# Performance work log

Measured on AMD Instinct MI355X. Metric: run time of the kernel, lower is better.

The kernel has to match this reference:

```python
import jax, jax.numpy as jnp
import numpy as np

GAMMA = 0.1
BUDGET = 64
EPS = 1e-8  # torch cosine_similarity clamp


def setup_inputs() -> dict:
    key = jax.random.key(0)
    k1, k2, k3, k4 = jax.random.split(key, 4)
    num_nodes, feat_dim, num_cand = 100000, 256, 50000
    return {
        "influence_scores": jax.random.normal(k1, (num_cand,), dtype=jnp.float32),
        "node_features": jax.random.normal(k2, (num_nodes, feat_dim), dtype=jnp.float32),
        "candidate_indices": jax.random.randint(k3, (num_cand,), 0, num_nodes, dtype=jnp.int64),
        "injected_feat": jax.random.normal(k4, (feat_dim,), dtype=jnp.float32),
    }


def reference(influence_scores, node_features, candidate_indices, injected_feat):
    # gather candidate features: [num_cand, feat_dim]
    cand_feat = node_features[candidate_indices]
    # cosine similarity vs injected_feat, torch-style eps clamp on norms
    inj_norm = jnp.maximum(jnp.linalg.norm(injected_feat), EPS)
    cand_norm = jnp.maximum(jnp.linalg.norm(cand_feat, axis=-1), EPS)
    sim_penalty = (cand_feat @ injected_feat) / (cand_norm * inj_norm)
    edge_scores = influence_scores - GAMMA * sim_penalty
    top_k = min(BUDGET, candidate_indices.shape[0])
    _, selected_indices = jax.lax.top_k(edge_scores, top_k)
    return candidate_indices[selected_indices], edge_scores
```

## Files before the change

kernel.cpp:

```cpp
#include <hip/hip_runtime.h>
#include <hip/hip_bf16.h>
#include <float.h>
#include <limits.h>

#define FEAT       256
#define GAMMA_F    0.1f
#define EPS_F      1e-8f
#define KSEL       64
#define NBUCK      4096
#define KSHIFT     20
#define NB1        1024
#define NB3        64
#define CPW        4
#define BCAP       64
#define CAP        4096
#define ZWORDS     (NBUCK + NB3 + 3)

__device__ __forceinline__ unsigned key_of(float v) {
    unsigned u = __float_as_uint(v);
    return u ^ ((u >> 31) ? 0xFFFFFFFFu : 0x80000000u);
}

__device__ __forceinline__ bool comes_first(float va, int ia, float vb, int ib) {
    return (va > vb) || (va == vb && ia < ib);
}

__global__ __launch_bounds__(256) void edge_score_kernel(
    const float* __restrict__ infl,
    const float* __restrict__ feats,
    const int*   __restrict__ cand,
    const float* __restrict__ inj,
    float*       __restrict__ scores,
    unsigned*    __restrict__ ws_zero,
    int num_cand)
{
    const int gtid = blockIdx.x * blockDim.x + threadIdx.x;
    if (gtid < ZWORDS) ws_zero[gtid] = 0u;

    const int lane    = threadIdx.x & 63;
    const int wid     = gtid >> 6;
    const int nwaves  = NB1 * 4;
    const int ngroups = (num_cand + CPW - 1) / CPW;

    const float4 g = *reinterpret_cast<const float4*>(inj + lane * 4);
    float ng = g.x * g.x + g.y * g.y + g.z * g.z + g.w * g.w;
    #pragma unroll
    for (int off = 32; off > 0; off >>= 1) ng += __shfl_xor(ng, off);
    const float inj_n = fmaxf(sqrtf(ng), EPS_F);

    for (int grp = wid; grp < ngroups; grp += nwaves) {
        const int base   = grp * CPW;
        const int n_here = num_cand - base;

        const int r0 = cand[base];
        const int r1 = (n_here > 1) ? cand[base + 1] : r0;
        const int r2 = (n_here > 2) ? cand[base + 2] : r0;
        const int r3 = (n_here > 3) ? cand[base + 3] : r0;
        const float4 f0 = *reinterpret_cast<const float4*>(feats + (size_t)r0 * FEAT + lane * 4);
        const float4 f1 = *reinterpret_cast<const float4*>(feats + (size_t)r1 * FEAT + lane * 4);
        const float4 f2 = *reinterpret_cast<const float4*>(feats + (size_t)r2 * FEAT + lane * 4);
        const float4 f3 = *reinterpret_cast<const float4*>(feats + (size_t)r3 * FEAT + lane * 4);

        float dot0 = f0.x*g.x + f0.y*g.y + f0.z*g.z + f0.w*g.w;
        float nf0  = f0.x*f0.x + f0.y*f0.y + f0.z*f0.z + f0.w*f0.w;
        float dot1 = f1.x*g.x + f1.y*g.y + f1.z*g.z + f1.w*g.w;
        float nf1  = f1.x*f1.x + f1.y*f1.y + f1.z*f1.z + f1.w*f1.w;
        float dot2 = f2.x*g.x + f2.y*g.y + f2.z*g.z + f2.w*g.w;
        float nf2  = f2.x*f2.x + f2.y*f2.y + f2.z*f2.z + f2.w*f2.w;
        float dot3 = f3.x*g.x + f3.y*g.y + f3.z*g.z + f3.w*g.w;
        float nf3  = f3.x*f3.x + f3.y*f3.y + f3.z*f3.z + f3.w*f3.w;

        #pragma unroll
        for (int off = 32; off > 0; off >>= 1) {
            dot0 += __shfl_xor(dot0, off);  nf0 += __shfl_xor(nf0, off);
            dot1 += __shfl_xor(dot1, off);  nf1 += __shfl_xor(nf1, off);
            dot2 += __shfl_xor(dot2, off);  nf2 += __shfl_xor(nf2, off);
            dot3 += __shfl_xor(dot3, off);  nf3 += __shfl_xor(nf3, off);
        }

        if (lane == 0) {
            const float s0 = infl[base] - GAMMA_F * (dot0 / (fmaxf(sqrtf(nf0), EPS_F) * inj_n));
            if (n_here >= 4) {
                const float s1 = infl[base+1] - GAMMA_F * (dot1 / (fmaxf(sqrtf(nf1), EPS_F) * inj_n));
                const float s2 = infl[base+2] - GAMMA_F * (dot2 / (fmaxf(sqrtf(nf2), EPS_F) * inj_n));
                const float s3 = infl[base+3] - GAMMA_F * (dot3 / (fmaxf(sqrtf(nf3), EPS_F) * inj_n));
                *reinterpret_cast<float4*>(scores + base) = make_float4(s0, s1, s2, s3);
            } else {
                scores[base] = s0;
                if (n_here > 1)
                    scores[base+1] = infl[base+1] - GAMMA_F * (dot1 / (fmaxf(sqrtf(nf1), EPS_F) * inj_n));
                if (n_here > 2)
                    scores[base+2] = infl[base+2] - GAMMA_F * (dot2 / (fmaxf(sqrtf(nf2), EPS_F) * inj_n));
            }
        }
    }
}

__global__ __launch_bounds__(256) void hist_kernel(
    const float* __restrict__ scores,
    unsigned*    __restrict__ hist,
    int n)
{
    __shared__ unsigned h[NBUCK];
    for (int i = threadIdx.x; i < NBUCK; i += 256) h[i] = 0;
    __syncthreads();

    const int n4 = n >> 2;
    const float4* s4 = reinterpret_cast<const float4*>(scores);
    for (int g = blockIdx.x * 256 + threadIdx.x; g < n4; g += NB3 * 256) {
        const float4 v = s4[g];
        atomicAdd(&h[key_of(v.x) >> KSHIFT], 1u);
        atomicAdd(&h[key_of(v.y) >> KSHIFT], 1u);
        atomicAdd(&h[key_of(v.z) >> KSHIFT], 1u);
        atomicAdd(&h[key_of(v.w) >> KSHIFT], 1u);
    }
    if (blockIdx.x == 0 && threadIdx.x < (n & 3))
        atomicAdd(&h[key_of(scores[n4 * 4 + threadIdx.x]) >> KSHIFT], 1u);
    __syncthreads();

    for (int i = threadIdx.x; i < NBUCK; i += 256)
        if (h[i]) atomicAdd(&hist[i], h[i]);
}

__global__ __launch_bounds__(256) void select_kernel(
    const float*    __restrict__ scores,
    const unsigned* __restrict__ hist,
    unsigned*       __restrict__ counts,
    unsigned*       __restrict__ done,
    unsigned*       __restrict__ oflow,
    float*          __restrict__ ws_v,
    int*            __restrict__ ws_i,
    const int*      __restrict__ cand,
    float*          __restrict__ out,
    int n)
{
    __shared__ unsigned csum[256];
    __shared__ unsigned sB, sCnt;
    __shared__ int      sLast;
    __shared__ unsigned soff[NB3 + 1];
    __shared__ float    sv[CAP];
    __shared__ int      si[CAP];

    const int t   = threadIdx.x;
    const int bid = blockIdx.x;

    {
        const int hi = NBUCK - 16 * t;
        unsigned s = 0;
        for (int b = hi - 16; b < hi; ++b) s += hist[b];
        csum[t] = s;
    }
    __syncthreads();
    if (t == 0) {
        unsigned cum = 0;
        int tc = 0;
        for (; tc < 256; ++tc) {
            if (cum + csum[tc] >= KSEL) break;
            cum += csum[tc];
        }
        unsigned B = 0;
        if (tc < 256) {
            int b = NBUCK - 16 * tc - 1;
            for (int k = 0; k < 16; ++k, --b) {
                cum += hist[b];
                if (cum >= KSEL) { B = (unsigned)b; break; }
            }
        }
        sB = B;
        sCnt = 0;
    }
    __syncthreads();
    const unsigned B = sB;

    const int n4 = n >> 2;
    const float4* s4 = reinterpret_cast<const float4*>(scores);
    for (int g = bid * 256 + t; g < n4; g += NB3 * 256) {
        const float4 v = s4[g];
        const float vv[4] = {v.x, v.y, v.z, v.w};
        #pragma unroll
        for (int j = 0; j < 4; ++j) {
            if ((key_of(vv[j]) >> KSHIFT) >= B) {
                const unsigned p = atomicAdd(&sCnt, 1u);
                if (p < BCAP) { ws_v[bid * BCAP + p] = vv[j]; ws_i[bid * BCAP + p] = g * 4 + j; }
            }
        }
    }
    if (bid == 0 && t < (n & 3)) {
        const float v = scores[n4 * 4 + t];
        if ((key_of(v) >> KSHIFT) >= B) {
            const unsigned p = atomicAdd(&sCnt, 1u);
            if (p < BCAP) { ws_v[p] = v; ws_i[p] = n4 * 4 + t; }
        }
    }
    __syncthreads();
    if (t == 0) {
        counts[bid] = min(sCnt, (unsigned)BCAP);
        if (sCnt > BCAP) atomicAdd(&oflow[0], 1u);
    }

    __threadfence();
    __syncthreads();
    if (t == 0) sLast = (atomicAdd(done, 1u) == (unsigned)(NB3 - 1));
    __syncthreads();
    if (!sLast) return;
    __threadfence();

    int m;
    if (oflow[0] == 0u) {
        if (t == 0) {
            unsigned acc = 0;
            #pragma unroll
            for (int r = 0; r < NB3; ++r) { soff[r] = acc; acc += counts[r]; }
            soff[NB3] = acc;
        }
        __syncthreads();
        m = (int)soff[NB3];
        for (int idx = t; idx < NB3 * BCAP; idx += 256) {
            const int r = idx >> 6, j = idx & (BCAP - 1);
            if ((unsigned)j < counts[r]) {
                const unsigned dst = soff[r] + j;
                sv[dst] = ws_v[r * BCAP + j];
                si[dst] = ws_i[r * BCAP + j];
            }
        }
    } else {
        if (t == 0) sCnt = 0;
        __syncthreads();
        for (int g = t; g < n; g += 256) {
            const float v = scores[g];
            if ((key_of(v) >> KSHIFT) >= B) {
                const unsigned p = atomicAdd(&sCnt, 1u);
                if (p < CAP) { sv[p] = v; si[p] = g; }
            }
        }
        __syncthreads();
        m = (int)min(sCnt, (unsigned)CAP);
    }
    __syncthreads();

    if (m <= 256) {
        if (t >= m) { sv[t] = -INFINITY; si[t] = INT_MAX; }
        __syncthreads();
        for (int k = 2; k <= 256; k <<= 1) {
            for (int j = k >> 1; j > 0; j >>= 1) {
                const int p = t ^ j;
                if (p > t) {
                    const float va = sv[t], vb = sv[p];
                    const int   ia = si[t], ib = si[p];
                    const bool asc = ((t & k) == 0);
                    const bool doSwap = asc ? comes_first(vb, ib, va, ia)
                                            : comes_first(va, ia, vb, ib);
                    if (doSwap) { sv[t] = vb; si[t] = ib; sv[p] = va; si[p] = ia; }
                }
                __syncthreads();
            }
        }
        if (t < KSEL) out[t] = (float)cand[si[t]];
        return;
    }

    __shared__ float wv[4];
    __shared__ int   wbi[4], wbs[4];
    for (int i = t + m; i < CAP; i += 256) { sv[i] = -INFINITY; si[i] = INT_MAX; }
    __syncthreads();
    for (int k = 0; k < KSEL; ++k) {
        float bv = -INFINITY; int bi = INT_MAX; int bs = 0;
        for (int i = t; i < CAP; i += 256) {
            if (comes_first(sv[i], si[i], bv, bi)) { bv = sv[i]; bi = si[i]; bs = i; }
        }
        #pragma unroll
        for (int off = 32; off > 0; off >>= 1) {
            const float ov = __shfl_xor(bv, off);
            const int   oi = __shfl_xor(bi, off);
            const int   os = __shfl_xor(bs, off);
            if (comes_first(ov, oi, bv, bi)) { bv = ov; bi = oi; bs = os; }
        }
        const int w = t >> 6;
        if ((t & 63) == 0) { wv[w] = bv; wbi[w] = bi; wbs[w] = bs; }
        __syncthreads();
        if (t == 0) {
            float fv = wv[0]; int fi = wbi[0]; int fs = wbs[0];
            #pragma unroll
            for (int j = 1; j < 4; ++j)
                if (comes_first(wv[j], wbi[j], fv, fi)) { fv = wv[j]; fi = wbi[j]; fs = wbs[j]; }
            out[k] = (float)cand[fi];
            sv[fs] = -INFINITY;
            si[fs] = INT_MAX;
        }
        __syncthreads();
    }
}

extern "C" void kernel_launch(void* const* d_in, const int* in_sizes, int n_in,
                              void* d_out, int out_size, void* d_ws, size_t ws_size,
                              hipStream_t stream) {
    const float* infl  = (const float*)d_in[0];
    const float* feats = (const float*)d_in[1];
    const int*   cand  = (const int*)d_in[2];
    const float* inj   = (const float*)d_in[3];

    const int num_cand = in_sizes[0];

    float* out    = (float*)d_out;
    float* scores = (float*)d_out + KSEL;

    unsigned* ws_hist   = (unsigned*)d_ws;
    unsigned* ws_counts = ws_hist + NBUCK;
    unsigned* ws_done   = ws_counts + NB3;
    unsigned* ws_oflow  = ws_done + 1;
    float*    ws_v      = (float*)(ws_oflow + 2);
    int*      ws_i      = (int*)(ws_v + NB3 * BCAP);

    edge_score_kernel<<<NB1, 256, 0, stream>>>(
        infl, feats, cand, inj, scores, ws_hist, num_cand);

    hist_kernel<<<NB3, 256, 0, stream>>>(scores, ws_hist, num_cand);

    select_kernel<<<NB3, 256, 0, stream>>>(
        scores, ws_hist, ws_counts, ws_done, ws_oflow, ws_v, ws_i, cand, out, num_cand);
}
```

Measured before the change: 46.33 us.

## Fuse histogram into scoring kernel with replicated global atomic histogram

Drops the separate histogram kernel. The scoring kernel now issues global atomics into a 16-way replicated histogram (replica chosen by wave id) as each score is produced, which spreads contention across copies. The select kernel sums the replicas when it picks the threshold bucket, and zeroing moves from in-kernel stores to a hipMemsetAsync. This saves one launch and one re-read of the scores, at the cost of per-score global atomics, a larger workspace to clear and more reads in select.

```diff
diff --git a/kernel.cpp b/kernel.cpp
--- a/kernel.cpp
+++ b/kernel.cpp
@@ -9,12 +9,12 @@
 #define KSEL       64
 #define NBUCK      4096
 #define KSHIFT     20
+#define NREP       16
 #define NB1        1024
 #define NB3        64
 #define CPW        4
 #define BCAP       64
 #define CAP        4096
-#define ZWORDS     (NBUCK + NB3 + 3)
 
 __device__ __forceinline__ unsigned key_of(float v) {
     unsigned u = __float_as_uint(v);
@@ -31,16 +31,15 @@
     const int*   __restrict__ cand,
     const float* __restrict__ inj,
     float*       __restrict__ scores,
-    unsigned*    __restrict__ ws_zero,
+    unsigned*    __restrict__ ghist,
     int num_cand)
 {
     const int gtid = blockIdx.x * blockDim.x + threadIdx.x;
-    if (gtid < ZWORDS) ws_zero[gtid] = 0u;
-
     const int lane    = threadIdx.x & 63;
     const int wid     = gtid >> 6;
     const int nwaves  = NB1 * 4;
     const int ngroups = (num_cand + CPW - 1) / CPW;
+    const int rep     = wid & (NREP - 1);
 
     const float4 g = *reinterpret_cast<const float4*>(inj + lane * 4);
     float ng = g.x * g.x + g.y * g.y + g.z * g.z + g.w * g.w;
@@ -85,46 +84,31 @@
                 const float s2 = infl[base+2] - GAMMA_F * (dot2 / (fmaxf(sqrtf(nf2), EPS_F) * inj_n));
                 const float s3 = infl[base+3] - GAMMA_F * (dot3 / (fmaxf(sqrtf(nf3), EPS_F) * inj_n));
                 *reinterpret_cast<float4*>(scores + base) = make_float4(s0, s1, s2, s3);
+                atomicAdd(&ghist[(key_of(s0) >> KSHIFT) * NREP + rep], 1u);
+                atomicAdd(&ghist[(key_of(s1) >> KSHIFT) * NREP + rep], 1u);
+                atomicAdd(&ghist[(key_of(s2) >> KSHIFT) * NREP + rep], 1u);
+                atomicAdd(&ghist[(key_of(s3) >> KSHIFT) * NREP + rep], 1u);
             } else {
                 scores[base] = s0;
-                if (n_here > 1)
-                    scores[base+1] = infl[base+1] - GAMMA_F * (dot1 / (fmaxf(sqrtf(nf1), EPS_F) * inj_n));
-                if (n_here > 2)
-                    scores[base+2] = infl[base+2] - GAMMA_F * (dot2 / (fmaxf(sqrtf(nf2), EPS_F) * inj_n));
-            }
-        }
-    }
-}
-
-__global__ __launch_bounds__(256) void hist_kernel(
-    const float* __restrict__ scores,
-    unsigned*    __restrict__ hist,
-    int n)
-{
-    __shared__ unsigned h[NBUCK];
-    for (int i = threadIdx.x; i < NBUCK; i += 256) h[i] = 0;
-    __syncthreads();
-
-    const int n4 = n >> 2;
-    const float4* s4 = reinterpret_cast<const float4*>(scores);
-    for (int g = blockIdx.x * 256 + threadIdx.x; g < n4; g += NB3 * 256) {
-        const float4 v = s4[g];
-        atomicAdd(&h[key_of(v.x) >> KSHIFT], 1u);
-        atomicAdd(&h[key_of(v.y) >> KSHIFT], 1u);
-        atomicAdd(&h[key_of(v.z) >> KSHIFT], 1u);
-        atomicAdd(&h[key_of(v.w) >> KSHIFT], 1u);
-    }
-    if (blockIdx.x == 0 && threadIdx.x < (n & 3))
-        atomicAdd(&h[key_of(scores[n4 * 4 + threadIdx.x]) >> KSHIFT], 1u);
-    __syncthreads();
-
-    for (int i = threadIdx.x; i < NBUCK; i += 256)
-        if (h[i]) atomicAdd(&hist[i], h[i]);
+                atomicAdd(&ghist[(key_of(s0) >> KSHIFT) * NREP + rep], 1u);
+                if (n_here > 1) {
+                    const float s1 = infl[base+1] - GAMMA_F * (dot1 / (fmaxf(sqrtf(nf1), EPS_F) * inj_n));
+                    scores[base+1] = s1;
+                    atomicAdd(&ghist[(key_of(s1) >> KSHIFT) * NREP + rep], 1u);
+                }
+                if (n_here > 2) {
+                    const float s2 = infl[base+2] - GAMMA_F * (dot2 / (fmaxf(sqrtf(nf2), EPS_F) * inj_n));
+                    scores[base+2] = s2;
+                    atomicAdd(&ghist[(key_of(s2) >> KSHIFT) * NREP + rep], 1u);
+                }
+            }
+        }
+    }
 }
 
 __global__ __launch_bounds__(256) void select_kernel(
     const float*    __restrict__ scores,
-    const unsigned* __restrict__ hist,
+    const unsigned* __restrict__ ghist,
     unsigned*       __restrict__ counts,
     unsigned*       __restrict__ done,
     unsigned*       __restrict__ oflow,
@@ -147,7 +131,14 @@
     {
         const int hi = NBUCK - 16 * t;
         unsigned s = 0;
-        for (int b = hi - 16; b < hi; ++b) s += hist[b];
+        for (int b = hi - 16; b < hi; ++b) {
+            const uint4* r4 = reinterpret_cast<const uint4*>(&ghist[b * NREP]);
+            #pragma unroll
+            for (int q = 0; q < NREP / 4; ++q) {
+                const uint4 a = r4[q];
+                s += a.x + a.y + a.z + a.w;
+            }
+        }
         csum[t] = s;
     }
     __syncthreads();
@@ -162,7 +153,10 @@
         if (tc < 256) {
             int b = NBUCK - 16 * tc - 1;
             for (int k = 0; k < 16; ++k, --b) {
-                cum += hist[b];
+                unsigned cb = 0;
+                #pragma unroll
+                for (int r = 0; r < NREP; ++r) cb += ghist[b * NREP + r];
+                cum += cb;
                 if (cum >= KSEL) { B = (unsigned)b; break; }
             }
         }
@@ -304,18 +298,18 @@
     float* out    = (float*)d_out;
     float* scores = (float*)d_out + KSEL;
 
-    unsigned* ws_hist   = (unsigned*)d_ws;
-    unsigned* ws_counts = ws_hist + NBUCK;
+    unsigned* ws_ghist  = (unsigned*)d_ws;
+    unsigned* ws_counts = ws_ghist + NBUCK * NREP;
     unsigned* ws_done   = ws_counts + NB3;
     unsigned* ws_oflow  = ws_done + 1;
     float*    ws_v      = (float*)(ws_oflow + 2);
     int*      ws_i      = (int*)(ws_v + NB3 * BCAP);
 
+    hipMemsetAsync(ws_ghist, 0, (NBUCK * NREP + NB3 + 3) * sizeof(unsigned), stream);
+
     edge_score_kernel<<<NB1, 256, 0, stream>>>(
-        infl, feats, cand, inj, scores, ws_hist, num_cand);
-
-    hist_kernel<<<NB3, 256, 0, stream>>>(scores, ws_hist, num_cand);
+        infl, feats, cand, inj, scores, ws_ghist, num_cand);
 
     select_kernel<<<NB3, 256, 0, stream>>>(
-        scores, ws_hist, ws_counts, ws_done, ws_oflow, ws_v, ws_i, cand, out, num_cand);
-}
+        scores, ws_ghist, ws_counts, ws_done, ws_oflow, ws_v, ws_i, cand, out, num_cand);
+}
```

Measured after the change: 73.98 us. +59.7%, slower.
